# Kernel optimization log

Measured on AMD Instinct MI355X. Metric: run time of the kernel, lower is better.

Reference implementation:

```python
import math
import jax, jax.numpy as jnp
import numpy as np

B, S, D, H = 2, 2048, 1024, 16
DH = D // H
DFF = 4 * D
EPS = 1e-6
MASKED_BIAS = -10000.0


def _gelu(x):
    # GPT-2 tanh-approx GELU
    return 0.5 * x * (1.0 + jnp.tanh(math.sqrt(2.0 / math.pi) * (x + 0.044715 * x ** 3)))


def _layernorm(x, w, b):
    mean = jnp.mean(x, axis=-1, keepdims=True)
    var = jnp.mean((x - mean) ** 2, axis=-1, keepdims=True)
    return w * ((x - mean) / jnp.sqrt(var + EPS)) + b


def setup_inputs() -> dict:
    key = jax.random.key(0)
    ks = jax.random.split(key, 6)
    std = 0.02
    return {
        "hidden_states": jax.random.normal(ks[0], (B, S, D), jnp.float32),
        "w_attn": jax.random.normal(ks[1], (D, 3 * D), jnp.float32) * std,
        "b_attn": jnp.zeros((3 * D,), jnp.float32),
        "w_proj": jax.random.normal(ks[2], (D, D), jnp.float32) * std,
        "b_proj": jnp.zeros((D,), jnp.float32),
        "w_fc": jax.random.normal(ks[3], (D, DFF), jnp.float32) * std,
        "b_fc": jnp.zeros((DFF,), jnp.float32),
        "w_fc_proj": jax.random.normal(ks[4], (DFF, D), jnp.float32) * std,
        "b_fc_proj": jnp.zeros((D,), jnp.float32),
        "ln1_w": jnp.ones((D,), jnp.float32),
        "ln1_b": jnp.zeros((D,), jnp.float32),
        "ln2_w": jnp.ones((D,), jnp.float32),
        "ln2_b": jnp.zeros((D,), jnp.float32),
    }


def reference(hidden_states, w_attn, b_attn, w_proj, b_proj, w_fc, b_fc,
              w_fc_proj, b_fc_proj, ln1_w, ln1_b, ln2_w, ln2_b):
    residual = hidden_states
    x = _layernorm(hidden_states, ln1_w, ln1_b)

    # c_attn: [B,S,D] @ [D,3D] + b -> split into q,k,v
    qkv = x @ w_attn + b_attn
    q, k, v = jnp.split(qkv, 3, axis=-1)
    # split heads -> [B,H,S,DH]
    q = q.reshape(B, S, H, DH).transpose(0, 2, 1, 3)
    k = k.reshape(B, S, H, DH).transpose(0, 2, 1, 3)
    v = v.reshape(B, S, H, DH).transpose(0, 2, 1, 3)

    scores = jnp.einsum('bhqd,bhkd->bhqk', q, k) / jnp.sqrt(jnp.float32(DH))
    causal = jnp.tril(jnp.ones((S, S), bool))  # [S,S]
    scores = jnp.where(causal[None, None], scores, jnp.float32(MASKED_BIAS))
    attn = jax.nn.softmax(scores, axis=-1)
    out = jnp.einsum('bhqk,bhkd->bhqd', attn, v)
    out = out.transpose(0, 2, 1, 3).reshape(B, S, D)
    out = out @ w_proj + b_proj

    h = residual + out
    residual = h
    y = _layernorm(h, ln2_w, ln2_b)
    y = _gelu(y @ w_fc + b_fc)
    y = y @ w_fc_proj + b_fc_proj
    return residual + y
```

## Files before the change

### kernel.cpp

```cpp
#include <hip/hip_runtime.h>
#include <cstdint>
#include <cstddef>

typedef unsigned short u16;
typedef float  floatx4 __attribute__((ext_vector_type(4)));
typedef short  short8  __attribute__((ext_vector_type(8)));
typedef u16    usx4    __attribute__((ext_vector_type(4)));
typedef u16    usx8    __attribute__((ext_vector_type(8)));

__device__ __forceinline__ u16 f2b(float f) {
  unsigned u = __float_as_uint(f);
  unsigned r = u + 0x7fffu + ((u >> 16) & 1u);
  return (u16)(r >> 16);
}
__device__ __forceinline__ float b2f(u16 s) {
  return __uint_as_float(((unsigned)s) << 16);
}

__device__ __forceinline__ float gelu_f(float x) {
  const float k = 2.3022082f;
  float u = x * (1.0f + 0.044715f * x * x);
  float t = __builtin_amdgcn_exp2f(-k * u);
  return x * __builtin_amdgcn_rcpf(1.0f + t);
}

__device__ __forceinline__ void gl2lds16(const u16* g, u16* l) {
  __builtin_amdgcn_global_load_lds(
      (const __attribute__((address_space(1))) unsigned int*)g,
      (__attribute__((address_space(3))) unsigned int*)l, 16, 0, 0);
}

#define C2SCALE 0.18033688011112042f

__global__ __launch_bounds__(256) void ln_bf16_kernel(
    const float* __restrict__ in, const float* __restrict__ w,
    const float* __restrict__ b, u16* __restrict__ out)
{
  const int row = blockIdx.x;
  const int t = threadIdx.x;
  const float* p = in + (size_t)row * 1024 + t * 4;
  floatx4 v = *(const floatx4*)p;
  float s  = v.x + v.y + v.z + v.w;
  float ss = v.x*v.x + v.y*v.y + v.z*v.z + v.w*v.w;
  #pragma unroll
  for (int m = 1; m < 64; m <<= 1) {
    s  += __shfl_xor(s,  m);
    ss += __shfl_xor(ss, m);
  }
  __shared__ float red[8];
  if ((t & 63) == 0) { red[(t >> 6)*2] = s; red[(t >> 6)*2 + 1] = ss; }
  __syncthreads();
  s  = red[0] + red[2] + red[4] + red[6];
  ss = red[1] + red[3] + red[5] + red[7];
  const float mean = s * (1.0f / 1024.0f);
  const float var  = ss * (1.0f / 1024.0f) - mean * mean;
  const float rstd = rsqrtf(var + 1e-6f);
  floatx4 wv = *(const floatx4*)(w + t * 4);
  floatx4 bv = *(const floatx4*)(b + t * 4);
  usx4 o = { f2b(wv.x * ((v.x - mean) * rstd) + bv.x),
             f2b(wv.y * ((v.y - mean) * rstd) + bv.y),
             f2b(wv.z * ((v.z - mean) * rstd) + bv.z),
             f2b(wv.w * ((v.w - mean) * rstd) + bv.w) };
  *(usx4*)(out + (size_t)row * 1024 + t * 4) = o;
}

__global__ __launch_bounds__(256) void wtrans_kernel(
    const float* __restrict__ in, u16* __restrict__ out, int K, int N)
{
  __shared__ u16 tile[32][33];
  const int n0 = blockIdx.x * 32, k0 = blockIdx.y * 32;
  const int tx = threadIdx.x & 31, ty = threadIdx.x >> 5;
  #pragma unroll
  for (int i = 0; i < 4; ++i)
    tile[ty + i*8][tx] = f2b(in[(size_t)(k0 + ty + i*8) * N + n0 + tx]);
  __syncthreads();
  #pragma unroll
  for (int i = 0; i < 4; ++i)
    out[(size_t)(n0 + ty + i*8) * K + k0 + tx] = tile[tx][ty + i*8];
}

template<int BM, int BN, int FLAGS, int MINW>
__global__ __launch_bounds__(256, MINW) void gemm_mfma_kernel(
    const u16* __restrict__ A, const u16* __restrict__ Bt,
    const float* __restrict__ bias, const float* __restrict__ Res,
    void* __restrict__ Cout, int M, int N, int K, int kLen, size_t zStride)
{
  constexpr int WM = BM / 2, WN = BN / 2;
  constexpr int MT = WM / 16, NT = WN / 16;
  __shared__ u16 As[BM * 32];
  __shared__ u16 Bs[BN * 32];

  const int t = threadIdx.x;
  const int wave = t >> 6, lane = t & 63;
  const int quad = lane >> 4, l16 = lane & 15;
  const int wm = wave >> 1, wn = wave & 1;
  const int bm0 = blockIdx.y * BM, bn0 = blockIdx.x * BN;
  const int kStart = blockIdx.z * kLen;

  const int sRow = lane >> 2;
  const int sq   = (lane & 3) ^ (sRow & 3);

  const u16* aG[BM / 64];
  u16* aL[BM / 64];
  #pragma unroll
  for (int j = 0; j < BM / 64; ++j) {
    const int band = j * 4 + wave;
    aG[j] = A + (size_t)(bm0 + band * 16 + sRow) * K + kStart + sq * 8;
    aL[j] = As + band * 512;
  }
  const u16* bG[BN / 64];
  u16* bL[BN / 64];
  #pragma unroll
  for (int j = 0; j < BN / 64; ++j) {
    const int band = j * 4 + wave;
    bG[j] = Bt + (size_t)(bn0 + band * 16 + sRow) * K + kStart + sq * 8;
    bL[j] = Bs + band * 512;
  }

  floatx4 acc[MT][NT] = {};
  const int rcol = (quad ^ (l16 & 3)) << 3;

  for (int k0 = 0; k0 < kLen; k0 += 32) {
    __syncthreads();
    #pragma unroll
    for (int j = 0; j < BM / 64; ++j) gl2lds16(aG[j] + k0, aL[j]);
    #pragma unroll
    for (int j = 0; j < BN / 64; ++j) gl2lds16(bG[j] + k0, bL[j]);
    __syncthreads();

    short8 af[MT], bf[NT];
    #pragma unroll
    for (int mt = 0; mt < MT; ++mt)
      af[mt] = *(const short8*)&As[(wm*WM + mt*16 + l16) * 32 + rcol];
    #pragma unroll
    for (int nt = 0; nt < NT; ++nt)
      bf[nt] = *(const short8*)&Bs[(wn*WN + nt*16 + l16) * 32 + rcol];
    #pragma unroll
    for (int mt = 0; mt < MT; ++mt)
      #pragma unroll
      for (int nt = 0; nt < NT; ++nt)
        acc[mt][nt] = __builtin_amdgcn_mfma_f32_16x16x32_bf16(af[mt], bf[nt], acc[mt][nt], 0, 0, 0);
  }

  const int orow0 = bm0 + wm * WM;
  const int ocol0 = bn0 + wn * WN;
  const size_t zoff = (size_t)blockIdx.z * zStride;
  #pragma unroll
  for (int nt = 0; nt < NT; ++nt) {
    const int col = ocol0 + nt*16 + l16;
    const float bv = bias ? bias[col] : 0.0f;
    const float postscale = ((FLAGS & 8) && col < 1024) ? C2SCALE : 1.0f;
    #pragma unroll
    for (int mt = 0; mt < MT; ++mt) {
      #pragma unroll
      for (int r = 0; r < 4; ++r) {
        const int row = orow0 + mt*16 + quad*4 + r;
        float v = acc[mt][nt][r] + bv;
        if (FLAGS & 1) v = gelu_f(v);
        if (FLAGS & 8) v *= postscale;
        if (FLAGS & 2) v += Res[(size_t)row * N + col];
        if (FLAGS & 4) ((u16*)Cout)[zoff + (size_t)row * N + col] = f2b(v);
        else           ((float*)Cout)[zoff + (size_t)row * N + col] = v;
      }
    }
  }
}

__global__ __launch_bounds__(256, 4) void attn_mfma_kernel(
    const u16* __restrict__ qkv, u16* __restrict__ opart, float* __restrict__ ml)
{
  __shared__ u16 Ks[64][72];
  __shared__ u16 Vt[64][72];
  __shared__ u16 Ps[64][72];

  const int t    = threadIdx.x;
  const int wave = t >> 6;
  const int lane = t & 63;
  const int quad = lane >> 4;
  const int l16  = lane & 15;
  const int pair = blockIdx.x >> 1;
  const int half = blockIdx.x & 1;
  const int h    = blockIdx.y;
  const int b    = blockIdx.z;

  const size_t base = (size_t)b * 2048 * 3072;
  const int qoff = h * 64;
  const int koff = 1024 + h * 64;
  const int voff = 2048 + h * 64;

  const int srow = t >> 2;
  const int scol = (t & 3) * 16;
  const int kpair  = t & 31;
  const int vchunk = t >> 5;

  const size_t obase  = ((((size_t)half * 2 + b) * 16 + h) * 2048) * 64;
  const size_t mlbase = ((((size_t)half * 2 + b) * 16 + h) * 2048) * 2;

  short8 onesb;
  {
    const short v = (l16 == 0) ? (short)0x3F80 : (short)0;
    #pragma unroll
    for (int i = 0; i < 8; ++i) onesb[i] = v;
  }

  #pragma unroll 1
  for (int iter = 0; iter < 2; ++iter) {
    const int qi = iter ? (31 - pair) : pair;
    const int q0 = qi << 6;
    const int T  = qi + 1;
    const int mid = (T + 1) >> 1;
    const int t0 = half ? mid : 0;
    const int t1 = half ? T : mid;

    floatx4 of[4] = {};
    floatx4 ofl = {};
    float m[4];
    #pragma unroll
    for (int r = 0; r < 4; ++r) m[r] = -1e30f;

    if (t0 < t1) {
      __syncthreads();
      {
        const u16* qp = qkv + base + (size_t)(q0 + srow) * 3072 + qoff + scol;
        *(usx8*)&Ks[srow][scol]     = *(const usx8*)qp;
        *(usx8*)&Ks[srow][scol + 8] = *(const usx8*)(qp + 8);
      }
      __syncthreads();
      const short8 qf0 = *(const short8*)&Ks[wave*16 + l16][quad*8];
      const short8 qf1 = *(const short8*)&Ks[wave*16 + l16][32 + quad*8];

      usx8 kr0, kr1, vr0, vr1;
      {
        const int k0 = t0 << 6;
        const u16* kp = qkv + base + (size_t)(k0 + srow) * 3072 + koff + scol;
        kr0 = *(const usx8*)kp; kr1 = *(const usx8*)(kp + 8);
        const u16* vp = qkv + base + (size_t)(k0 + 2*kpair) * 3072 + voff + vchunk*8;
        vr0 = *(const usx8*)vp; vr1 = *(const usx8*)(vp + 3072);
      }

      for (int tIdx = t0; tIdx < t1; ++tIdx) {
        __syncthreads();
        *(usx8*)&Ks[srow][scol]     = kr0;
        *(usx8*)&Ks[srow][scol + 8] = kr1;
        #pragma unroll
        for (int i = 0; i < 8; ++i)
          *(unsigned*)&Vt[vchunk*8 + i][2*kpair] =
              (unsigned)vr0[i] | ((unsigned)vr1[i] << 16);
        __syncthreads();

        if (tIdx + 1 < t1) {
          const int kn = (tIdx + 1) << 6;
          const u16* kp = qkv + base + (size_t)(kn + srow) * 3072 + koff + scol;
          kr0 = *(const usx8*)kp; kr1 = *(const usx8*)(kp + 8);
          const u16* vp = qkv + base + (size_t)(kn + 2*kpair) * 3072 + voff + vchunk*8;
          vr0 = *(const usx8*)vp; vr1 = *(const usx8*)(vp + 3072);
        }

        const int k0 = tIdx << 6;
        floatx4 sf[4];
        #pragma unroll
        for (int kt = 0; kt < 4; ++kt) {
          short8 kf0 = *(const short8*)&Ks[kt*16 + l16][quad*8];
          short8 kf1 = *(const short8*)&Ks[kt*16 + l16][32 + quad*8];
          floatx4 z = {};
          z      = __builtin_amdgcn_mfma_f32_16x16x32_bf16(qf0, kf0, z, 0, 0, 0);
          sf[kt] = __builtin_amdgcn_mfma_f32_16x16x32_bf16(qf1, kf1, z, 0, 0, 0);
        }

        const bool diag = (tIdx == qi);
        #pragma unroll
        for (int r = 0; r < 4; ++r) {
          float sv0 = sf[0][r], sv1 = sf[1][r], sv2 = sf[2][r], sv3 = sf[3][r];
          if (diag) {
            const int qrow = q0 + wave*16 + quad*4 + r;
            if (k0 +      l16 > qrow) sv0 = -1e30f;
            if (k0 + 16 + l16 > qrow) sv1 = -1e30f;
            if (k0 + 32 + l16 > qrow) sv2 = -1e30f;
            if (k0 + 48 + l16 > qrow) sv3 = -1e30f;
          }
          float mx = fmaxf(fmaxf(sv0, sv1), fmaxf(sv2, sv3));
          #pragma unroll
          for (int msk = 1; msk < 16; msk <<= 1) mx = fmaxf(mx, __shfl_xor(mx, msk, 16));
          const float nm = fmaxf(m[r], mx);
          const float alpha = exp2f(m[r] - nm);
          m[r] = nm;
          Ps[wave*16 + quad*4 + r][     l16] = f2b(exp2f(sv0 - nm));
          Ps[wave*16 + quad*4 + r][16 + l16] = f2b(exp2f(sv1 - nm));
          Ps[wave*16 + quad*4 + r][32 + l16] = f2b(exp2f(sv2 - nm));
          Ps[wave*16 + quad*4 + r][48 + l16] = f2b(exp2f(sv3 - nm));
          #pragma unroll
          for (int dht = 0; dht < 4; ++dht) of[dht][r] *= alpha;
          ofl[r] *= alpha;
        }

        short8 pf0 = *(const short8*)&Ps[wave*16 + l16][quad*8];
        short8 pf1 = *(const short8*)&Ps[wave*16 + l16][32 + quad*8];
        #pragma unroll
        for (int dht = 0; dht < 4; ++dht) {
          short8 vf0 = *(const short8*)&Vt[dht*16 + l16][quad*8];
          short8 vf1 = *(const short8*)&Vt[dht*16 + l16][32 + quad*8];
          of[dht] = __builtin_amdgcn_mfma_f32_16x16x32_bf16(pf0, vf0, of[dht], 0, 0, 0);
          of[dht] = __builtin_amdgcn_mfma_f32_16x16x32_bf16(pf1, vf1, of[dht], 0, 0, 0);
        }
        ofl = __builtin_amdgcn_mfma_f32_16x16x32_bf16(pf0, onesb, ofl, 0, 0, 0);
        ofl = __builtin_amdgcn_mfma_f32_16x16x32_bf16(pf1, onesb, ofl, 0, 0, 0);
      }
    }

    #pragma unroll
    for (int r = 0; r < 4; ++r) {
      const int s = q0 + wave*16 + quad*4 + r;
      u16* orow = opart + obase + (size_t)s * 64;
      #pragma unroll
      for (int dht = 0; dht < 4; ++dht) orow[dht*16 + l16] = f2b(of[dht][r]);
      const float lr = __shfl(ofl[r], quad * 16);
      if (l16 == 0) { ml[mlbase + 2*s] = m[r]; ml[mlbase + 2*s + 1] = lr; }
    }
  }
}

__global__ __launch_bounds__(256) void attn_combine_kernel(
    const u16* __restrict__ opart, const float* __restrict__ ml,
    u16* __restrict__ out)
{
  const int t = threadIdx.x;
  const int s = blockIdx.x * 4 + (t >> 6);
  const int lane = t & 63;
  const int h = blockIdx.y, b = blockIdx.z;

  const size_t o0  = ((((size_t)0 * 2 + b) * 16 + h) * 2048 + s) * 64 + lane;
  const size_t o1  = ((((size_t)1 * 2 + b) * 16 + h) * 2048 + s) * 64 + lane;
  const size_t ml0 = ((((size_t)0 * 2 + b) * 16 + h) * 2048 + s) * 2;
  const size_t ml1 = ((((size_t)1 * 2 + b) * 16 + h) * 2048 + s) * 2;

  const float m0 = ml[ml0], l0 = ml[ml0 + 1];
  const float m1 = ml[ml1], l1 = ml[ml1 + 1];
  const float M  = fmaxf(m0, m1);
  const float w0 = exp2f(m0 - M), w1 = exp2f(m1 - M);
  const float L  = w0 * l0 + w1 * l1;
  const float o  = w0 * b2f(opart[o0]) + w1 * b2f(opart[o1]);
  out[((size_t)b * 2048 + s) * 1024 + h * 64 + lane] = f2b(o / L);
}

__global__ __launch_bounds__(256) void ksplit_combine_kernel(
    const u16* __restrict__ p0, const u16* __restrict__ p1,
    const float* __restrict__ res, const float* __restrict__ bias,
    float* __restrict__ out)
{
  const size_t i0 = ((size_t)blockIdx.x * 256 + threadIdx.x) * 8;
  usx8 a = *(const usx8*)(p0 + i0);
  usx8 c = *(const usx8*)(p1 + i0);
  const int col = (int)(i0 & 1023);
  floatx4 bv0 = *(const floatx4*)(bias + col);
  floatx4 bv1 = *(const floatx4*)(bias + col + 4);
  floatx4 h0 = *(const floatx4*)(res + i0);
  floatx4 h1 = *(const floatx4*)(res + i0 + 4);
  floatx4 o0, o1;
  #pragma unroll
  for (int i = 0; i < 4; ++i) o0[i] = h0[i] + b2f(a[i])   + b2f(c[i])   + bv0[i];
  #pragma unroll
  for (int i = 0; i < 4; ++i) o1[i] = h1[i] + b2f(a[4+i]) + b2f(c[4+i]) + bv1[i];
  *(floatx4*)(out + i0)     = o0;
  *(floatx4*)(out + i0 + 4) = o1;
}

extern "C" void kernel_launch(void* const* d_in, const int* in_sizes, int n_in,
                              void* d_out, int out_size, void* d_ws, size_t ws_size,
                              hipStream_t stream) {
  const float* hidden    = (const float*)d_in[0];
  const float* w_attn    = (const float*)d_in[1];
  const float* b_attn    = (const float*)d_in[2];
  const float* w_proj    = (const float*)d_in[3];
  const float* b_proj    = (const float*)d_in[4];
  const float* w_fc      = (const float*)d_in[5];
  const float* b_fc      = (const float*)d_in[6];
  const float* w_fc_proj = (const float*)d_in[7];
  const float* b_fc_proj = (const float*)d_in[8];
  const float* ln1_w     = (const float*)d_in[9];
  const float* ln1_b     = (const float*)d_in[10];
  const float* ln2_w     = (const float*)d_in[11];
  const float* ln2_b     = (const float*)d_in[12];

  char* wsb = (char*)d_ws;
  u16*   qkvb  = (u16*)  (wsb + (size_t)( 0u << 20));
  u16*   xb    = (u16*)  (wsb + (size_t)(24u << 20));
  u16*   opart = (u16*)  (wsb + (size_t)(24u << 20));
  float* mlbuf = (float*)(wsb + (size_t)(40u << 20));
  u16*   attnb = (u16*)  (wsb + (size_t)(42u << 20));
  u16*   wqT   = (u16*)  (wsb + (size_t)(50u << 20));
  u16*   wpT   = (u16*)  (wsb + (size_t)(56u << 20));
  u16*   wfT   = (u16*)  (wsb + (size_t)(58u << 20));
  u16*   wfpT  = (u16*)  (wsb + (size_t)(66u << 20));
  u16*   pproj = (u16*)  (wsb + (size_t)(24u << 20));
  float* hbuf  = (float*)(wsb + (size_t)(42u << 20));
  u16*   yb    = (u16*)  (wsb + (size_t)( 0u << 20));
  u16*   fcb   = (u16*)  (wsb + (size_t)( 8u << 20));
  u16*   pfcp0 = (u16*)  (wsb + (size_t)( 0u << 20));
  u16*   pfcp1 = (u16*)  (wsb + (size_t)(58u << 20));
  const size_t zstr_fcp = ((size_t)58u << 20) / 2;

  wtrans_kernel<<<dim3(96, 32),  256, 0, stream>>>(w_attn,    wqT,  1024, 3072);
  wtrans_kernel<<<dim3(32, 32),  256, 0, stream>>>(w_proj,    wpT,  1024, 1024);
  wtrans_kernel<<<dim3(128, 32), 256, 0, stream>>>(w_fc,      wfT,  1024, 4096);
  wtrans_kernel<<<dim3(32, 128), 256, 0, stream>>>(w_fc_proj, wfpT, 4096, 1024);

  ln_bf16_kernel<<<4096, 256, 0, stream>>>(hidden, ln1_w, ln1_b, xb);
  gemm_mfma_kernel<128,128,12,4><<<dim3(24, 32, 1), 256, 0, stream>>>(
      xb, wqT, b_attn, nullptr, qkvb, 4096, 3072, 1024, 1024, 0);
  attn_mfma_kernel<<<dim3(32, 16, 2), 256, 0, stream>>>(qkvb, opart, mlbuf);
  attn_combine_kernel<<<dim3(512, 16, 2), 256, 0, stream>>>(opart, mlbuf, attnb);
  gemm_mfma_kernel<128,64,4,4><<<dim3(16, 32, 2), 256, 0, stream>>>(
      attnb, wpT, nullptr, nullptr, pproj, 4096, 1024, 1024, 512, 4194304);
  ksplit_combine_kernel<<<dim3(2048), 256, 0, stream>>>(
      pproj, pproj + 4194304, hidden, b_proj, hbuf);
  ln_bf16_kernel<<<4096, 256, 0, stream>>>(hbuf, ln2_w, ln2_b, yb);
  gemm_mfma_kernel<128,128,5,4><<<dim3(32, 32, 1), 256, 0, stream>>>(
      yb, wfT, b_fc, nullptr, fcb, 4096, 4096, 1024, 1024, 0);
  gemm_mfma_kernel<128,64,4,4><<<dim3(16, 32, 2), 256, 0, stream>>>(
      fcb, wfpT, nullptr, nullptr, pfcp0, 4096, 1024, 4096, 2048, zstr_fcp);
  ksplit_combine_kernel<<<dim3(2048), 256, 0, stream>>>(
      pfcp0, pfcp1, hbuf, b_fc_proj, (float*)d_out);
}
```

Measured before the change: 382.2 us.

## Fuse weight transposes, fuse split-K combine with LN2, vectorize attention P stores

Merges the four weight-transpose launches into one kernel and fuses the attention-projection split-K combine with the second layernorm, so the residual sum feeds normalization without a separate launch and re-read. In the attention kernel, K rows are loaded in a permuted order so each lane's four score columns are contiguous. This lets the bf16 probabilities be packed and written to LDS as one 8-byte store, and the causal mask is adjusted to match. It also switches exp2f to the raw hardware exp2 intrinsic, trading some edge-case accuracy handling for fewer instructions.

```diff
diff --git a/kernel.cpp b/kernel.cpp
--- a/kernel.cpp
+++ b/kernel.cpp
@@ -7,6 +7,7 @@
 typedef short  short8  __attribute__((ext_vector_type(8)));
 typedef u16    usx4    __attribute__((ext_vector_type(4)));
 typedef u16    usx8    __attribute__((ext_vector_type(8)));
+typedef unsigned uintx2 __attribute__((ext_vector_type(2)));
 
 __device__ __forceinline__ u16 f2b(float f) {
   unsigned u = __float_as_uint(f);
@@ -64,12 +65,54 @@
   *(usx4*)(out + (size_t)row * 1024 + t * 4) = o;
 }
 
-__global__ __launch_bounds__(256) void wtrans_kernel(
-    const float* __restrict__ in, u16* __restrict__ out, int K, int N)
+__global__ __launch_bounds__(256) void combine_ln_kernel(
+    const u16* __restrict__ p0, const u16* __restrict__ p1,
+    const float* __restrict__ res, const float* __restrict__ bias,
+    const float* __restrict__ w, const float* __restrict__ b,
+    float* __restrict__ hout, u16* __restrict__ yout)
+{
+  const int row = blockIdx.x;
+  const int t = threadIdx.x;
+  const size_t i0 = (size_t)row * 1024 + t * 4;
+  floatx4 rv = *(const floatx4*)(res + i0);
+  usx4 a = *(const usx4*)(p0 + i0);
+  usx4 c = *(const usx4*)(p1 + i0);
+  floatx4 biasv = *(const floatx4*)(bias + t * 4);
+  floatx4 v;
+  #pragma unroll
+  for (int i = 0; i < 4; ++i) v[i] = rv[i] + b2f(a[i]) + b2f(c[i]) + biasv[i];
+  *(floatx4*)(hout + i0) = v;
+
+  float s  = v.x + v.y + v.z + v.w;
+  float ss = v.x*v.x + v.y*v.y + v.z*v.z + v.w*v.w;
+  #pragma unroll
+  for (int m = 1; m < 64; m <<= 1) {
+    s  += __shfl_xor(s,  m);
+    ss += __shfl_xor(ss, m);
+  }
+  __shared__ float red[8];
+  if ((t & 63) == 0) { red[(t >> 6)*2] = s; red[(t >> 6)*2 + 1] = ss; }
+  __syncthreads();
+  s  = red[0] + red[2] + red[4] + red[6];
+  ss = red[1] + red[3] + red[5] + red[7];
+  const float mean = s * (1.0f / 1024.0f);
+  const float var  = ss * (1.0f / 1024.0f) - mean * mean;
+  const float rstd = rsqrtf(var + 1e-6f);
+  floatx4 wv = *(const floatx4*)(w + t * 4);
+  floatx4 bv = *(const floatx4*)(b + t * 4);
+  usx4 o = { f2b(wv.x * ((v.x - mean) * rstd) + bv.x),
+             f2b(wv.y * ((v.y - mean) * rstd) + bv.y),
+             f2b(wv.z * ((v.z - mean) * rstd) + bv.z),
+             f2b(wv.w * ((v.w - mean) * rstd) + bv.w) };
+  *(usx4*)(yout + i0) = o;
+}
+
+__device__ __forceinline__ void wtrans_body(
+    const float* __restrict__ in, u16* __restrict__ out, int K, int N,
+    int bx, int by, int tx, int ty)
 {
   __shared__ u16 tile[32][33];
-  const int n0 = blockIdx.x * 32, k0 = blockIdx.y * 32;
-  const int tx = threadIdx.x & 31, ty = threadIdx.x >> 5;
+  const int n0 = bx * 32, k0 = by * 32;
   #pragma unroll
   for (int i = 0; i < 4; ++i)
     tile[ty + i*8][tx] = f2b(in[(size_t)(k0 + ty + i*8) * N + n0 + tx]);
@@ -77,6 +120,25 @@
   #pragma unroll
   for (int i = 0; i < 4; ++i)
     out[(size_t)(n0 + ty + i*8) * K + k0 + tx] = tile[tx][ty + i*8];
+}
+
+__global__ __launch_bounds__(256) void wtrans4_kernel(
+    const float* __restrict__ w0, const float* __restrict__ w1,
+    const float* __restrict__ w2, const float* __restrict__ w3,
+    u16* __restrict__ o0, u16* __restrict__ o1,
+    u16* __restrict__ o2, u16* __restrict__ o3)
+{
+  int blk = blockIdx.x;
+  const int tx = threadIdx.x & 31, ty = threadIdx.x >> 5;
+  if (blk < 3072) {
+    wtrans_body(w0, o0, 1024, 3072, blk % 96, blk / 96, tx, ty);
+  } else if (blk < 4096) {
+    blk -= 3072; wtrans_body(w1, o1, 1024, 1024, blk % 32, blk / 32, tx, ty);
+  } else if (blk < 8192) {
+    blk -= 4096; wtrans_body(w2, o2, 1024, 4096, blk % 128, blk / 128, tx, ty);
+  } else {
+    blk -= 8192; wtrans_body(w3, o3, 4096, 1024, blk % 32, blk / 32, tx, ty);
+  }
 }
 
 template<int BM, int BN, int FLAGS, int MINW>
@@ -188,8 +250,9 @@
   const int koff = 1024 + h * 64;
   const int voff = 2048 + h * 64;
 
-  const int srow = t >> 2;
+  const int prow = t >> 2;
   const int scol = (t & 3) * 16;
+  const int kmap = ((prow & 15) << 2) | (prow >> 4);
   const int kpair  = t & 31;
   const int vchunk = t >> 5;
 
@@ -221,9 +284,9 @@
     if (t0 < t1) {
       __syncthreads();
       {
-        const u16* qp = qkv + base + (size_t)(q0 + srow) * 3072 + qoff + scol;
-        *(usx8*)&Ks[srow][scol]     = *(const usx8*)qp;
-        *(usx8*)&Ks[srow][scol + 8] = *(const usx8*)(qp + 8);
+        const u16* qp = qkv + base + (size_t)(q0 + prow) * 3072 + qoff + scol;
+        *(usx8*)&Ks[prow][scol]     = *(const usx8*)qp;
+        *(usx8*)&Ks[prow][scol + 8] = *(const usx8*)(qp + 8);
       }
       __syncthreads();
       const short8 qf0 = *(const short8*)&Ks[wave*16 + l16][quad*8];
@@ -232,7 +295,7 @@
       usx8 kr0, kr1, vr0, vr1;
       {
         const int k0 = t0 << 6;
-        const u16* kp = qkv + base + (size_t)(k0 + srow) * 3072 + koff + scol;
+        const u16* kp = qkv + base + (size_t)(k0 + kmap) * 3072 + koff + scol;
         kr0 = *(const usx8*)kp; kr1 = *(const usx8*)(kp + 8);
         const u16* vp = qkv + base + (size_t)(k0 + 2*kpair) * 3072 + voff + vchunk*8;
         vr0 = *(const usx8*)vp; vr1 = *(const usx8*)(vp + 3072);
@@ -240,8 +303,8 @@
 
       for (int tIdx = t0; tIdx < t1; ++tIdx) {
         __syncthreads();
-        *(usx8*)&Ks[srow][scol]     = kr0;
-        *(usx8*)&Ks[srow][scol + 8] = kr1;
+        *(usx8*)&Ks[prow][scol]     = kr0;
+        *(usx8*)&Ks[prow][scol + 8] = kr1;
         #pragma unroll
         for (int i = 0; i < 8; ++i)
           *(unsigned*)&Vt[vchunk*8 + i][2*kpair] =
@@ -250,7 +313,7 @@
 
         if (tIdx + 1 < t1) {
           const int kn = (tIdx + 1) << 6;
-          const u16* kp = qkv + base + (size_t)(kn + srow) * 3072 + koff + scol;
+          const u16* kp = qkv + base + (size_t)(kn + kmap) * 3072 + koff + scol;
           kr0 = *(const usx8*)kp; kr1 = *(const usx8*)(kp + 8);
           const u16* vp = qkv + base + (size_t)(kn + 2*kpair) * 3072 + voff + vchunk*8;
           vr0 = *(const usx8*)vp; vr1 = *(const usx8*)(vp + 3072);
@@ -273,21 +336,24 @@
           float sv0 = sf[0][r], sv1 = sf[1][r], sv2 = sf[2][r], sv3 = sf[3][r];
           if (diag) {
             const int qrow = q0 + wave*16 + quad*4 + r;
-            if (k0 +      l16 > qrow) sv0 = -1e30f;
-            if (k0 + 16 + l16 > qrow) sv1 = -1e30f;
-            if (k0 + 32 + l16 > qrow) sv2 = -1e30f;
-            if (k0 + 48 + l16 > qrow) sv3 = -1e30f;
+            const int kbase = k0 + 4*l16;
+            if (kbase     > qrow) sv0 = -1e30f;
+            if (kbase + 1 > qrow) sv1 = -1e30f;
+            if (kbase + 2 > qrow) sv2 = -1e30f;
+            if (kbase + 3 > qrow) sv3 = -1e30f;
           }
           float mx = fmaxf(fmaxf(sv0, sv1), fmaxf(sv2, sv3));
           #pragma unroll
           for (int msk = 1; msk < 16; msk <<= 1) mx = fmaxf(mx, __shfl_xor(mx, msk, 16));
           const float nm = fmaxf(m[r], mx);
-          const float alpha = exp2f(m[r] - nm);
+          const float alpha = __builtin_amdgcn_exp2f(m[r] - nm);
           m[r] = nm;
-          Ps[wave*16 + quad*4 + r][     l16] = f2b(exp2f(sv0 - nm));
-          Ps[wave*16 + quad*4 + r][16 + l16] = f2b(exp2f(sv1 - nm));
-          Ps[wave*16 + quad*4 + r][32 + l16] = f2b(exp2f(sv2 - nm));
-          Ps[wave*16 + quad*4 + r][48 + l16] = f2b(exp2f(sv3 - nm));
+          const unsigned e0 = f2b(__builtin_amdgcn_exp2f(sv0 - nm));
+          const unsigned e1 = f2b(__builtin_amdgcn_exp2f(sv1 - nm));
+          const unsigned e2 = f2b(__builtin_amdgcn_exp2f(sv2 - nm));
+          const unsigned e3 = f2b(__builtin_amdgcn_exp2f(sv3 - nm));
+          uintx2 pw = { e0 | (e1 << 16), e2 | (e3 << 16) };
+          *(uintx2*)&Ps[wave*16 + quad*4 + r][l16 * 4] = pw;
           #pragma unroll
           for (int dht = 0; dht < 4; ++dht) of[dht][r] *= alpha;
           ofl[r] *= alpha;
@@ -336,7 +402,8 @@
   const float m0 = ml[ml0], l0 = ml[ml0 + 1];
   const float m1 = ml[ml1], l1 = ml[ml1 + 1];
   const float M  = fmaxf(m0, m1);
-  const float w0 = exp2f(m0 - M), w1 = exp2f(m1 - M);
+  const float w0 = __builtin_amdgcn_exp2f(m0 - M);
+  const float w1 = __builtin_amdgcn_exp2f(m1 - M);
   const float L  = w0 * l0 + w1 * l1;
   const float o  = w0 * b2f(opart[o0]) + w1 * b2f(opart[o1]);
   out[((size_t)b * 2048 + s) * 1024 + h * 64 + lane] = f2b(o / L);
@@ -399,10 +466,8 @@
   u16*   pfcp1 = (u16*)  (wsb + (size_t)(58u << 20));
   const size_t zstr_fcp = ((size_t)58u << 20) / 2;
 
-  wtrans_kernel<<<dim3(96, 32),  256, 0, stream>>>(w_attn,    wqT,  1024, 3072);
-  wtrans_kernel<<<dim3(32, 32),  256, 0, stream>>>(w_proj,    wpT,  1024, 1024);
-  wtrans_kernel<<<dim3(128, 32), 256, 0, stream>>>(w_fc,      wfT,  1024, 4096);
-  wtrans_kernel<<<dim3(32, 128), 256, 0, stream>>>(w_fc_proj, wfpT, 4096, 1024);
+  wtrans4_kernel<<<dim3(12288), 256, 0, stream>>>(
+      w_attn, w_proj, w_fc, w_fc_proj, wqT, wpT, wfT, wfpT);
 
   ln_bf16_kernel<<<4096, 256, 0, stream>>>(hidden, ln1_w, ln1_b, xb);
   gemm_mfma_kernel<128,128,12,4><<<dim3(24, 32, 1), 256, 0, stream>>>(
@@ -411,9 +476,8 @@
   attn_combine_kernel<<<dim3(512, 16, 2), 256, 0, stream>>>(opart, mlbuf, attnb);
   gemm_mfma_kernel<128,64,4,4><<<dim3(16, 32, 2), 256, 0, stream>>>(
       attnb, wpT, nullptr, nullptr, pproj, 4096, 1024, 1024, 512, 4194304);
-  ksplit_combine_kernel<<<dim3(2048), 256, 0, stream>>>(
-      pproj, pproj + 4194304, hidden, b_proj, hbuf);
-  ln_bf16_kernel<<<4096, 256, 0, stream>>>(hbuf, ln2_w, ln2_b, yb);
+  combine_ln_kernel<<<4096, 256, 0, stream>>>(
+      pproj, pproj + 4194304, hidden, b_proj, ln2_w, ln2_b, hbuf, yb);
   gemm_mfma_kernel<128,128,5,4><<<dim3(32, 32, 1), 256, 0, stream>>>(
       yb, wfT, b_fc, nullptr, fcb, 4096, 4096, 1024, 1024, 0);
   gemm_mfma_kernel<128,64,4,4><<<dim3(16, 32, 2), 256, 0, stream>>>(
```

Measured after the change: 364.1 us. 1.05x faster.
